# Kernel optimization log

Hardware: AMD Instinct MI355X
Metric: run time of the kernel (lower is better)

## Reference

```python
import jax, jax.numpy as jnp
import numpy as np

LN_EPS = 1e-5


def setup_inputs() -> dict:
    key = jax.random.key(0)
    ks = jax.random.split(key, 10)
    N, E, D, H = 32000, 512000, 256, 128
    atom_features = jax.random.normal(ks[0], (N, D), dtype=jnp.float32)
    edge_features = jax.random.normal(ks[1], (E, H), dtype=jnp.float32)
    edge_index = jax.random.randint(ks[2], (2, E), 0, N, dtype=jnp.int64)
    s = lambda fan_in: 1.0 / np.sqrt(fan_in)
    W_lin = jax.random.normal(ks[3], (D, H), dtype=jnp.float32) * s(D)
    W1 = jax.random.normal(ks[4], (3 * H, H), dtype=jnp.float32) * s(3 * H)
    b1 = jnp.zeros((H,), jnp.float32)
    W2 = jax.random.normal(ks[5], (H, H), dtype=jnp.float32) * s(H)
    b2 = jnp.zeros((H,), jnp.float32)
    W3 = jax.random.normal(ks[6], (H, H), dtype=jnp.float32) * s(H)
    b3 = jnp.zeros((H,), jnp.float32)
    gamma = jnp.ones((H,), jnp.float32)
    beta = jnp.zeros((H,), jnp.float32)
    return dict(atom_features=atom_features, edge_features=edge_features,
                edge_index=edge_index, W_lin=W_lin, W1=W1, b1=b1, W2=W2,
                b2=b2, W3=W3, b3=b3, gamma=gamma, beta=beta)


def _layernorm(x, gamma, beta):
    mu = jnp.mean(x, axis=-1, keepdims=True)
    var = jnp.mean((x - mu) ** 2, axis=-1, keepdims=True)
    return (x - mu) * jax.lax.rsqrt(var + LN_EPS) * gamma + beta


def reference(atom_features, edge_features, edge_index, W_lin, W1, b1, W2, b2, W3, b3, gamma, beta):
    # o3.Linear on scalar irreps -> plain bias-free linear: [N, D] @ [D, H]
    atom_scalars = atom_features @ W_lin  # [N, H]
    edge_dst, edge_src = edge_index[0], edge_index[1]
    # gather + concat: [E, 3H]
    edge_in = jnp.concatenate(
        [atom_scalars[edge_dst], atom_scalars[edge_src], edge_features], axis=-1)
    h = jax.nn.relu(edge_in @ W1 + b1)
    h = jax.nn.relu(h @ W2 + b2)
    h = h @ W3 + b3  # [E, H]
    return _layernorm(edge_features + h, gamma, beta)
```

## Files before the change

kernel.cpp:

```cpp
#include <hip/hip_runtime.h>

typedef __attribute__((ext_vector_type(8))) short bf16x8;
typedef __attribute__((ext_vector_type(16))) float f32x16;

#define LN_EPS 1e-5f

__device__ __forceinline__ unsigned short f2bf(float f) {
    unsigned u = __float_as_uint(f);
    unsigned r = (u + 0x7FFFu + ((u >> 16) & 1u)) >> 16;
    return (unsigned short)r;
}

__global__ void prep_weights(const float* __restrict__ W_lin,
                             const float* __restrict__ W1,
                             const float* __restrict__ W2,
                             const float* __restrict__ W3,
                             unsigned short* __restrict__ wt_lin,
                             unsigned short* __restrict__ wt5) {
    int i = blockIdx.x * blockDim.x + threadIdx.x;
    if (i < 128 * 256) {
        int n = i >> 8, k = i & 255;
        wt_lin[n * 256 + k] = f2bf(W_lin[k * 128 + n]);
    } else if (i < 128 * 256 + 5 * 128 * 128) {
        int j = i - 128 * 256;
        int m = j >> 14, r = j & 16383;
        int n = r >> 7, k = r & 127;
        float v;
        if (m < 3)       v = W1[(m * 128 + k) * 128 + n];
        else if (m == 3) v = W2[k * 128 + n];
        else             v = W3[k * 128 + n];
        int kk = k ^ ((n & 7) << 3);
        wt5[m * 16384 + n * 128 + kk] = f2bf(v);
    }
}

__global__ void atoms_gemm(const float* __restrict__ af,
                           const unsigned short* __restrict__ wt_lin,
                           unsigned short* __restrict__ atoms_bf,
                           int Natoms) {
    const int wv = threadIdx.x >> 6, lane = threadIdx.x & 63;
    const int l31 = lane & 31, g8 = (lane >> 5) * 8, g4 = (lane >> 5) * 4;
    const int R = blockIdx.x * 128 + wv * 32;

    f32x16 acc[4];
#pragma unroll
    for (int f = 0; f < 4; ++f)
#pragma unroll
        for (int e = 0; e < 16; ++e) acc[f][e] = 0.0f;

    int arow = R + l31;
    if (arow >= Natoms) arow = Natoms - 1;
    const float* ap = af + (size_t)arow * 256;

#pragma unroll
    for (int ks = 0; ks < 16; ++ks) {
        const int k0 = ks * 16 + g8;
        float4 x0 = *(const float4*)(ap + k0);
        float4 x1 = *(const float4*)(ap + k0 + 4);
        bf16x8 a;
        a[0] = (short)f2bf(x0.x); a[1] = (short)f2bf(x0.y);
        a[2] = (short)f2bf(x0.z); a[3] = (short)f2bf(x0.w);
        a[4] = (short)f2bf(x1.x); a[5] = (short)f2bf(x1.y);
        a[6] = (short)f2bf(x1.z); a[7] = (short)f2bf(x1.w);
#pragma unroll
        for (int f = 0; f < 4; ++f) {
            bf16x8 b = *(const bf16x8*)(wt_lin + (32 * f + l31) * 256 + k0);
            acc[f] = __builtin_amdgcn_mfma_f32_32x32x16_bf16(a, b, acc[f], 0, 0, 0);
        }
    }

#pragma unroll
    for (int f = 0; f < 4; ++f) {
        const int col = 32 * f + l31;
#pragma unroll
        for (int r = 0; r < 16; ++r) {
            int row = R + (r & 3) + 8 * (r >> 2) + g4;
            if (row < Natoms) atoms_bf[(size_t)row * 128 + col] = f2bf(acc[f][r]);
        }
    }
}

__device__ __forceinline__ void zero4(f32x16* a) {
#pragma unroll
    for (int f = 0; f < 4; ++f)
#pragma unroll
        for (int e = 0; e < 16; ++e) a[f][e] = 0.0f;
}

__device__ __forceinline__ void chunk_globalA(const unsigned short* __restrict__ arow,
                                              const unsigned short* __restrict__ W,
                                              int l31, int g8, int sw, f32x16* acc) {
#pragma unroll
    for (int ks = 0; ks < 8; ++ks) {
        bf16x8 a = *(const bf16x8*)(arow + ks * 16 + g8);
#pragma unroll
        for (int f = 0; f < 4; ++f) {
            bf16x8 b = *(const bf16x8*)(W + (32 * f + l31) * 128 + ((ks * 16 + g8) ^ sw));
            acc[f] = __builtin_amdgcn_mfma_f32_32x32x16_bf16(a, b, acc[f], 0, 0, 0);
        }
    }
}

__device__ __forceinline__ void chunk_ldsA(const unsigned short* __restrict__ actw,
                                           const unsigned short* __restrict__ W,
                                           int l31, int g8, int sw, f32x16* acc) {
#pragma unroll
    for (int ks = 0; ks < 8; ++ks) {
        bf16x8 a = *(const bf16x8*)(actw + l31 * 128 + ((ks * 16 + g8) ^ sw));
#pragma unroll
        for (int f = 0; f < 4; ++f) {
            bf16x8 b = *(const bf16x8*)(W + (32 * f + l31) * 128 + ((ks * 16 + g8) ^ sw));
            acc[f] = __builtin_amdgcn_mfma_f32_32x32x16_bf16(a, b, acc[f], 0, 0, 0);
        }
    }
}

__global__ __launch_bounds__(512, 2) void edge_mlp(
    const float* __restrict__ ef, const int* __restrict__ eidx,
    const unsigned short* __restrict__ atoms_bf,
    const unsigned short* __restrict__ wt5,
    const float* __restrict__ b1, const float* __restrict__ b2,
    const float* __restrict__ b3, const float* __restrict__ gamma_,
    const float* __restrict__ beta_, float* __restrict__ out, int E) {
    __shared__ unsigned short Wbuf[2][16384];
    __shared__ unsigned short act[8][4096];

    const int tid = threadIdx.x;
    const int wv = tid >> 6, lane = tid & 63;
    const int l31 = lane & 31, g = lane >> 5, g8 = g * 8, g4 = g * 4;
    const int sw = (l31 & 7) << 3;
    const int R = blockIdx.x * 256 + wv * 32;

    auto stage = [&](int buf, int mat) {
        const char* s = (const char*)(wt5 + mat * 16384);
        char* d = (char*)(&Wbuf[buf][0]);
        const int o = tid * 16;
#pragma unroll
        for (int i = 0; i < 4; ++i)
            __builtin_amdgcn_global_load_lds(
                (const __attribute__((address_space(1))) unsigned int*)(s + o + i * 8192),
                (__attribute__((address_space(3))) unsigned int*)(d + o + i * 8192),
                16, 0, 0);
    };

    int e_l = R + l31;
    if (e_l >= E) e_l = E - 1;
    const int dstI = eidx[e_l];
    const int srcI = eidx[E + e_l];

    float b1c[4], b2c[4], b3c[4], gc[4], bc[4];
#pragma unroll
    for (int f = 0; f < 4; ++f) {
        const int c = 32 * f + l31;
        b1c[f] = b1[c]; b2c[f] = b2[c]; b3c[f] = b3[c];
        gc[f] = gamma_[c]; bc[f] = beta_[c];
    }

    unsigned short* actw = &act[wv][0];
    f32x16 acc[4];

    stage(0, 0);
    __syncthreads();

    zero4(acc);
    stage(1, 1);
    chunk_globalA(atoms_bf + (size_t)dstI * 128, &Wbuf[0][0], l31, g8, sw, acc);
    __syncthreads();

    stage(0, 2);
    chunk_globalA(atoms_bf + (size_t)srcI * 128, &Wbuf[1][0], l31, g8, sw, acc);
    __syncthreads();

    stage(1, 3);
    {
        const float* erow = ef + (size_t)e_l * 128;
        const unsigned short* W = &Wbuf[0][0];
#pragma unroll
        for (int ks = 0; ks < 8; ++ks) {
            const int k0 = ks * 16 + g8;
            float4 x0 = *(const float4*)(erow + k0);
            float4 x1 = *(const float4*)(erow + k0 + 4);
            bf16x8 a;
            a[0] = (short)f2bf(x0.x); a[1] = (short)f2bf(x0.y);
            a[2] = (short)f2bf(x0.z); a[3] = (short)f2bf(x0.w);
            a[4] = (short)f2bf(x1.x); a[5] = (short)f2bf(x1.y);
            a[6] = (short)f2bf(x1.z); a[7] = (short)f2bf(x1.w);
#pragma unroll
            for (int f = 0; f < 4; ++f) {
                bf16x8 b = *(const bf16x8*)(W + (32 * f + l31) * 128 + (k0 ^ sw));
                acc[f] = __builtin_amdgcn_mfma_f32_32x32x16_bf16(a, b, acc[f], 0, 0, 0);
            }
        }
    }
#pragma unroll
    for (int f = 0; f < 4; ++f) {
        const int col = 32 * f + l31;
#pragma unroll
        for (int r = 0; r < 16; ++r) {
            const int row = (r & 3) + 8 * (r >> 2) + g4;
            float v = fmaxf(acc[f][r] + b1c[f], 0.0f);
            actw[row * 128 + (col ^ ((row & 7) << 3))] = f2bf(v);
        }
    }
    __syncthreads();

    stage(0, 4);
    zero4(acc);
    chunk_ldsA(actw, &Wbuf[1][0], l31, g8, sw, acc);
#pragma unroll
    for (int f = 0; f < 4; ++f) {
        const int col = 32 * f + l31;
#pragma unroll
        for (int r = 0; r < 16; ++r) {
            const int row = (r & 3) + 8 * (r >> 2) + g4;
            float v = fmaxf(acc[f][r] + b2c[f], 0.0f);
            actw[row * 128 + (col ^ ((row & 7) << 3))] = f2bf(v);
        }
    }
    __syncthreads();

    zero4(acc);
    chunk_ldsA(actw, &Wbuf[0][0], l31, g8, sw, acc);

    float s_[16], q_[16];
#pragma unroll
    for (int r = 0; r < 16; ++r) { s_[r] = 0.0f; q_[r] = 0.0f; }
#pragma unroll
    for (int f = 0; f < 4; ++f) {
#pragma unroll
        for (int r = 0; r < 16; ++r) {
            int row = R + (r & 3) + 8 * (r >> 2) + g4;
            if (row >= E) row = E - 1;
            float v = acc[f][r] + b3c[f] + ef[(size_t)row * 128 + 32 * f + l31];
            acc[f][r] = v;
            s_[r] += v;
            q_[r] += v * v;
        }
    }
#pragma unroll
    for (int m = 1; m <= 16; m <<= 1) {
#pragma unroll
        for (int r = 0; r < 16; ++r) {
            s_[r] += __shfl_xor(s_[r], m, 64);
            q_[r] += __shfl_xor(q_[r], m, 64);
        }
    }
#pragma unroll
    for (int r = 0; r < 16; ++r) {
        const float mu = s_[r] * (1.0f / 128.0f);
        const float var = q_[r] * (1.0f / 128.0f) - mu * mu;
        const float rs = rsqrtf(var + LN_EPS);
        const int row = R + (r & 3) + 8 * (r >> 2) + g4;
        if (row < E) {
#pragma unroll
            for (int f = 0; f < 4; ++f)
                out[(size_t)row * 128 + 32 * f + l31] =
                    (acc[f][r] - mu) * rs * gc[f] + bc[f];
        }
    }
}

extern "C" void kernel_launch(void* const* d_in, const int* in_sizes, int n_in,
                              void* d_out, int out_size, void* d_ws, size_t ws_size,
                              hipStream_t stream) {
    const float* atom_features = (const float*)d_in[0];
    const float* edge_features = (const float*)d_in[1];
    const int* edge_index = (const int*)d_in[2];
    const float* W_lin = (const float*)d_in[3];
    const float* W1 = (const float*)d_in[4];
    const float* b1 = (const float*)d_in[5];
    const float* W2 = (const float*)d_in[6];
    const float* b2 = (const float*)d_in[7];
    const float* W3 = (const float*)d_in[8];
    const float* b3 = (const float*)d_in[9];
    const float* gamma_ = (const float*)d_in[10];
    const float* beta_ = (const float*)d_in[11];
    float* out = (float*)d_out;

    const int Natoms = in_sizes[0] / 256;
    const int E = in_sizes[1] / 128;

    unsigned short* atoms_bf = (unsigned short*)d_ws;
    unsigned short* wt_lin = atoms_bf + (size_t)Natoms * 128;
    unsigned short* wt5 = wt_lin + 128 * 256;

    const int prep_items = 128 * 256 + 5 * 128 * 128;
    prep_weights<<<(prep_items + 255) / 256, 256, 0, stream>>>(W_lin, W1, W2, W3,
                                                               wt_lin, wt5);
    atoms_gemm<<<(Natoms + 127) / 128, 256, 0, stream>>>(atom_features, wt_lin,
                                                         atoms_bf, Natoms);
    edge_mlp<<<(E + 255) / 256, 512, 0, stream>>>(edge_features, edge_index,
                                                  atoms_bf, wt5, b1, b2, b3,
                                                  gamma_, beta_, out, E);
}
```

Before: 267.5 us.

## Transpose edge MLP so activations stay in registers, weights read from pre-tiled global image

The edge MLP now computes the transposed product, with weights as the A operand and edge rows as B. Each lane's accumulator then holds a full edge row, so inter-layer activations are rebuilt in registers using packed bf16 conversion and permlane32 swaps instead of going through LDS, and the LayerNorm reduction needs a single cross-half shuffle. Weights are pre-arranged into a fragment-ordered image and read directly from global/L2 rather than staged into LDS with barriers. Blocks shrink to 256 threads with three blocks per CU, and output stores become vectorized float4. The risks are higher register pressure and repeated global weight reads per wave.

```diff
diff --git a/kernel.cpp b/kernel.cpp
--- a/kernel.cpp
+++ b/kernel.cpp
@@ -2,6 +2,8 @@
 
 typedef __attribute__((ext_vector_type(8))) short bf16x8;
 typedef __attribute__((ext_vector_type(16))) float f32x16;
+typedef __attribute__((ext_vector_type(4))) float f32x4;
+typedef __attribute__((ext_vector_type(4))) unsigned u32x4;
 
 #define LN_EPS 1e-5f
 
@@ -9,6 +11,16 @@
     unsigned u = __float_as_uint(f);
     unsigned r = (u + 0x7FFFu + ((u >> 16) & 1u)) >> 16;
     return (unsigned short)r;
+}
+
+__device__ __forceinline__ unsigned cvt_pk_bf16(float lo, float hi) {
+    unsigned r;
+    asm("v_cvt_pk_bf16_f32 %0, %1, %2" : "=v"(r) : "v"(lo), "v"(hi));
+    return r;
+}
+
+__device__ __forceinline__ void permswap(unsigned& a, unsigned& b) {
+    asm("v_permlane32_swap_b32 %0, %1" : "+v"(a), "+v"(b));
 }
 
 __global__ void prep_weights(const float* __restrict__ W_lin,
@@ -16,21 +28,22 @@
                              const float* __restrict__ W2,
                              const float* __restrict__ W3,
                              unsigned short* __restrict__ wt_lin,
-                             unsigned short* __restrict__ wt5) {
+                             unsigned short* __restrict__ wimg) {
     int i = blockIdx.x * blockDim.x + threadIdx.x;
     if (i < 128 * 256) {
         int n = i >> 8, k = i & 255;
         wt_lin[n * 256 + k] = f2bf(W_lin[k * 128 + n]);
-    } else if (i < 128 * 256 + 5 * 128 * 128) {
+    } else if (i < 128 * 256 + 5 * 16384) {
         int j = i - 128 * 256;
-        int m = j >> 14, r = j & 16383;
-        int n = r >> 7, k = r & 127;
+        int mat = j >> 14, r = j & 16383;
+        int jj = r & 7, l = (r >> 3) & 63, ks = (r >> 9) & 7, f = r >> 12;
+        int n = 32 * f + (l & 31);
+        int k = 16 * ks + 8 * (l >> 5) + jj;
         float v;
-        if (m < 3)       v = W1[(m * 128 + k) * 128 + n];
-        else if (m == 3) v = W2[k * 128 + n];
-        else             v = W3[k * 128 + n];
-        int kk = k ^ ((n & 7) << 3);
-        wt5[m * 16384 + n * 128 + kk] = f2bf(v);
+        if (mat < 3)       v = W1[(mat * 128 + k) * 128 + n];
+        else if (mat == 3) v = W2[k * 128 + n];
+        else               v = W3[k * 128 + n];
+        wimg[j + mat * 0 + (j - r) * 0 + (mat * 16384 + r) - j] = f2bf(v);
     }
 }
 
@@ -80,183 +93,155 @@
     }
 }
 
-__device__ __forceinline__ void zero4(f32x16* a) {
-#pragma unroll
-    for (int f = 0; f < 4; ++f)
-#pragma unroll
-        for (int e = 0; e < 16; ++e) a[f][e] = 0.0f;
-}
-
-__device__ __forceinline__ void chunk_globalA(const unsigned short* __restrict__ arow,
-                                              const unsigned short* __restrict__ W,
-                                              int l31, int g8, int sw, f32x16* acc) {
-#pragma unroll
-    for (int ks = 0; ks < 8; ++ks) {
-        bf16x8 a = *(const bf16x8*)(arow + ks * 16 + g8);
-#pragma unroll
-        for (int f = 0; f < 4; ++f) {
-            bf16x8 b = *(const bf16x8*)(W + (32 * f + l31) * 128 + ((ks * 16 + g8) ^ sw));
-            acc[f] = __builtin_amdgcn_mfma_f32_32x32x16_bf16(a, b, acc[f], 0, 0, 0);
-        }
-    }
-}
-
-__device__ __forceinline__ void chunk_ldsA(const unsigned short* __restrict__ actw,
-                                           const unsigned short* __restrict__ W,
-                                           int l31, int g8, int sw, f32x16* acc) {
-#pragma unroll
-    for (int ks = 0; ks < 8; ++ks) {
-        bf16x8 a = *(const bf16x8*)(actw + l31 * 128 + ((ks * 16 + g8) ^ sw));
-#pragma unroll
-        for (int f = 0; f < 4; ++f) {
-            bf16x8 b = *(const bf16x8*)(W + (32 * f + l31) * 128 + ((ks * 16 + g8) ^ sw));
-            acc[f] = __builtin_amdgcn_mfma_f32_32x32x16_bf16(a, b, acc[f], 0, 0, 0);
-        }
-    }
-}
-
-__global__ __launch_bounds__(512, 2) void edge_mlp(
+__global__ __launch_bounds__(256, 3) void edge_fused(
     const float* __restrict__ ef, const int* __restrict__ eidx,
     const unsigned short* __restrict__ atoms_bf,
-    const unsigned short* __restrict__ wt5,
+    const unsigned short* __restrict__ wimg,
     const float* __restrict__ b1, const float* __restrict__ b2,
     const float* __restrict__ b3, const float* __restrict__ gamma_,
     const float* __restrict__ beta_, float* __restrict__ out, int E) {
-    __shared__ unsigned short Wbuf[2][16384];
-    __shared__ unsigned short act[8][4096];
-
-    const int tid = threadIdx.x;
-    const int wv = tid >> 6, lane = tid & 63;
-    const int l31 = lane & 31, g = lane >> 5, g8 = g * 8, g4 = g * 4;
-    const int sw = (l31 & 7) << 3;
-    const int R = blockIdx.x * 256 + wv * 32;
-
-    auto stage = [&](int buf, int mat) {
-        const char* s = (const char*)(wt5 + mat * 16384);
-        char* d = (char*)(&Wbuf[buf][0]);
-        const int o = tid * 16;
-#pragma unroll
-        for (int i = 0; i < 4; ++i)
-            __builtin_amdgcn_global_load_lds(
-                (const __attribute__((address_space(1))) unsigned int*)(s + o + i * 8192),
-                (__attribute__((address_space(3))) unsigned int*)(d + o + i * 8192),
-                16, 0, 0);
+    const int lane = threadIdx.x & 63;
+    const int wv = threadIdx.x >> 6;
+    const int l31 = lane & 31;
+    const int hi = lane >> 5;
+    const int h8 = hi * 8;
+
+    const int e0 = blockIdx.x * 128 + wv * 32 + l31;
+    const int e = e0 < E ? e0 : E - 1;
+    const int dstI = eidx[e];
+    const int srcI = eidx[E + e];
+    const unsigned short* dstRow = atoms_bf + (size_t)dstI * 128;
+    const unsigned short* srcRow = atoms_bf + (size_t)srcI * 128;
+    const float* efRow = ef + (size_t)e * 128;
+
+    const unsigned short* wbase = wimg + lane * 8;
+
+    f32x16 acc[4];
+
+    auto initb = [&](const float* __restrict__ bb) {
+#pragma unroll
+        for (int f = 0; f < 4; ++f)
+#pragma unroll
+            for (int m = 0; m < 4; ++m) {
+                f32x4 b4 = *(const f32x4*)(bb + 32 * f + 8 * m + 4 * hi);
+#pragma unroll
+                for (int i = 0; i < 4; ++i) acc[f][4 * m + i] = b4[i];
+            }
     };
 
-    int e_l = R + l31;
-    if (e_l >= E) e_l = E - 1;
-    const int dstI = eidx[e_l];
-    const int srcI = eidx[E + e_l];
-
-    float b1c[4], b2c[4], b3c[4], gc[4], bc[4];
-#pragma unroll
-    for (int f = 0; f < 4; ++f) {
-        const int c = 32 * f + l31;
-        b1c[f] = b1[c]; b2c[f] = b2[c]; b3c[f] = b3[c];
-        gc[f] = gamma_[c]; bc[f] = beta_[c];
-    }
-
-    unsigned short* actw = &act[wv][0];
-    f32x16 acc[4];
-
-    stage(0, 0);
-    __syncthreads();
-
-    zero4(acc);
-    stage(1, 1);
-    chunk_globalA(atoms_bf + (size_t)dstI * 128, &Wbuf[0][0], l31, g8, sw, acc);
-    __syncthreads();
-
-    stage(0, 2);
-    chunk_globalA(atoms_bf + (size_t)srcI * 128, &Wbuf[1][0], l31, g8, sw, acc);
-    __syncthreads();
-
-    stage(1, 3);
-    {
-        const float* erow = ef + (size_t)e_l * 128;
-        const unsigned short* W = &Wbuf[0][0];
-#pragma unroll
-        for (int ks = 0; ks < 8; ++ks) {
-            const int k0 = ks * 16 + g8;
-            float4 x0 = *(const float4*)(erow + k0);
-            float4 x1 = *(const float4*)(erow + k0 + 4);
-            bf16x8 a;
-            a[0] = (short)f2bf(x0.x); a[1] = (short)f2bf(x0.y);
-            a[2] = (short)f2bf(x0.z); a[3] = (short)f2bf(x0.w);
-            a[4] = (short)f2bf(x1.x); a[5] = (short)f2bf(x1.y);
-            a[6] = (short)f2bf(x1.z); a[7] = (short)f2bf(x1.w);
-#pragma unroll
-            for (int f = 0; f < 4; ++f) {
-                bf16x8 b = *(const bf16x8*)(W + (32 * f + l31) * 128 + (k0 ^ sw));
-                acc[f] = __builtin_amdgcn_mfma_f32_32x32x16_bf16(a, b, acc[f], 0, 0, 0);
-            }
-        }
-    }
-#pragma unroll
-    for (int f = 0; f < 4; ++f) {
-        const int col = 32 * f + l31;
-#pragma unroll
-        for (int r = 0; r < 16; ++r) {
-            const int row = (r & 3) + 8 * (r >> 2) + g4;
-            float v = fmaxf(acc[f][r] + b1c[f], 0.0f);
-            actw[row * 128 + (col ^ ((row & 7) << 3))] = f2bf(v);
-        }
-    }
-    __syncthreads();
-
-    stage(0, 4);
-    zero4(acc);
-    chunk_ldsA(actw, &Wbuf[1][0], l31, g8, sw, acc);
-#pragma unroll
-    for (int f = 0; f < 4; ++f) {
-        const int col = 32 * f + l31;
-#pragma unroll
-        for (int r = 0; r < 16; ++r) {
-            const int row = (r & 3) + 8 * (r >> 2) + g4;
-            float v = fmaxf(acc[f][r] + b2c[f], 0.0f);
-            actw[row * 128 + (col ^ ((row & 7) << 3))] = f2bf(v);
-        }
-    }
-    __syncthreads();
-
-    zero4(acc);
-    chunk_ldsA(actw, &Wbuf[0][0], l31, g8, sw, acc);
-
-    float s_[16], q_[16];
-#pragma unroll
-    for (int r = 0; r < 16; ++r) { s_[r] = 0.0f; q_[r] = 0.0f; }
-#pragma unroll
-    for (int f = 0; f < 4; ++f) {
-#pragma unroll
-        for (int r = 0; r < 16; ++r) {
-            int row = R + (r & 3) + 8 * (r >> 2) + g4;
-            if (row >= E) row = E - 1;
-            float v = acc[f][r] + b3c[f] + ef[(size_t)row * 128 + 32 * f + l31];
-            acc[f][r] = v;
-            s_[r] += v;
-            q_[r] += v * v;
-        }
-    }
-#pragma unroll
-    for (int m = 1; m <= 16; m <<= 1) {
-#pragma unroll
-        for (int r = 0; r < 16; ++r) {
-            s_[r] += __shfl_xor(s_[r], m, 64);
-            q_[r] += __shfl_xor(q_[r], m, 64);
-        }
-    }
-#pragma unroll
-    for (int r = 0; r < 16; ++r) {
-        const float mu = s_[r] * (1.0f / 128.0f);
-        const float var = q_[r] * (1.0f / 128.0f) - mu * mu;
-        const float rs = rsqrtf(var + LN_EPS);
-        const int row = R + (r & 3) + 8 * (r >> 2) + g4;
-        if (row < E) {
-#pragma unroll
-            for (int f = 0; f < 4; ++f)
-                out[(size_t)row * 128 + 32 * f + l31] =
-                    (acc[f][r] - mu) * rs * gc[f] + bc[f];
-        }
+    bf16x8 frag[8];
+    auto build_frags = [&]() {
+#pragma unroll
+        for (int f = 0; f < 4; ++f) {
+            unsigned pk0[4], pk1[4];
+#pragma unroll
+            for (int m = 0; m < 4; ++m) {
+                float a0 = fmaxf(acc[f][4 * m + 0], 0.0f);
+                float a1 = fmaxf(acc[f][4 * m + 1], 0.0f);
+                float a2 = fmaxf(acc[f][4 * m + 2], 0.0f);
+                float a3 = fmaxf(acc[f][4 * m + 3], 0.0f);
+                pk0[m] = cvt_pk_bf16(a0, a1);
+                pk1[m] = cvt_pk_bf16(a2, a3);
+            }
+#pragma unroll
+            for (int k1 = 0; k1 < 2; ++k1) {
+                unsigned x0 = pk0[2 * k1], y0 = pk0[2 * k1 + 1];
+                unsigned x1 = pk1[2 * k1], y1 = pk1[2 * k1 + 1];
+                permswap(x0, y0);
+                permswap(x1, y1);
+                union { u32x4 u; bf16x8 b; } cv;
+                cv.u = (u32x4){x0, x1, y0, y1};
+                frag[2 * f + k1] = cv.b;
+            }
+        }
+    };
+
+    initb(b1);
+#pragma unroll
+    for (int ks = 0; ks < 8; ++ks) {
+        bf16x8 bx = *(const bf16x8*)(dstRow + ks * 16 + h8);
+#pragma unroll
+        for (int f = 0; f < 4; ++f) {
+            bf16x8 a = *(const bf16x8*)(wbase + ((0 * 4 + f) * 8 + ks) * 512);
+            acc[f] = __builtin_amdgcn_mfma_f32_32x32x16_bf16(a, bx, acc[f], 0, 0, 0);
+        }
+    }
+#pragma unroll
+    for (int ks = 0; ks < 8; ++ks) {
+        bf16x8 bx = *(const bf16x8*)(srcRow + ks * 16 + h8);
+#pragma unroll
+        for (int f = 0; f < 4; ++f) {
+            bf16x8 a = *(const bf16x8*)(wbase + ((1 * 4 + f) * 8 + ks) * 512);
+            acc[f] = __builtin_amdgcn_mfma_f32_32x32x16_bf16(a, bx, acc[f], 0, 0, 0);
+        }
+    }
+#pragma unroll
+    for (int ks = 0; ks < 8; ++ks) {
+        f32x4 x0 = *(const f32x4*)(efRow + ks * 16 + h8);
+        f32x4 x1 = *(const f32x4*)(efRow + ks * 16 + h8 + 4);
+        union { u32x4 u; bf16x8 b; } cv;
+        cv.u = (u32x4){cvt_pk_bf16(x0[0], x0[1]), cvt_pk_bf16(x0[2], x0[3]),
+                       cvt_pk_bf16(x1[0], x1[1]), cvt_pk_bf16(x1[2], x1[3])};
+#pragma unroll
+        for (int f = 0; f < 4; ++f) {
+            bf16x8 a = *(const bf16x8*)(wbase + ((2 * 4 + f) * 8 + ks) * 512);
+            acc[f] = __builtin_amdgcn_mfma_f32_32x32x16_bf16(a, cv.b, acc[f], 0, 0, 0);
+        }
+    }
+
+    build_frags();
+    initb(b2);
+#pragma unroll
+    for (int ks = 0; ks < 8; ++ks)
+#pragma unroll
+        for (int f = 0; f < 4; ++f) {
+            bf16x8 a = *(const bf16x8*)(wbase + ((3 * 4 + f) * 8 + ks) * 512);
+            acc[f] = __builtin_amdgcn_mfma_f32_32x32x16_bf16(a, frag[ks], acc[f], 0, 0, 0);
+        }
+
+    build_frags();
+    initb(b3);
+#pragma unroll
+    for (int ks = 0; ks < 8; ++ks)
+#pragma unroll
+        for (int f = 0; f < 4; ++f) {
+            bf16x8 a = *(const bf16x8*)(wbase + ((4 * 4 + f) * 8 + ks) * 512);
+            acc[f] = __builtin_amdgcn_mfma_f32_32x32x16_bf16(a, frag[ks], acc[f], 0, 0, 0);
+        }
+
+    float s = 0.0f, q = 0.0f;
+#pragma unroll
+    for (int f = 0; f < 4; ++f)
+#pragma unroll
+        for (int m = 0; m < 4; ++m) {
+            f32x4 r4 = *(const f32x4*)(efRow + 32 * f + 8 * m + 4 * hi);
+#pragma unroll
+            for (int i = 0; i < 4; ++i) {
+                float v = acc[f][4 * m + i] + r4[i];
+                acc[f][4 * m + i] = v;
+                s += v;
+                q += v * v;
+            }
+        }
+    s += __shfl_xor(s, 32, 64);
+    q += __shfl_xor(q, 32, 64);
+    const float mu = s * (1.0f / 128.0f);
+    const float var = q * (1.0f / 128.0f) - mu * mu;
+    const float rs = rsqrtf(var + LN_EPS);
+
+    if (e0 < E) {
+#pragma unroll
+        for (int f = 0; f < 4; ++f)
+#pragma unroll
+            for (int m = 0; m < 4; ++m) {
+                f32x4 g4 = *(const f32x4*)(gamma_ + 32 * f + 8 * m + 4 * hi);
+                f32x4 be4 = *(const f32x4*)(beta_ + 32 * f + 8 * m + 4 * hi);
+                f32x4 o;
+#pragma unroll
+                for (int i = 0; i < 4; ++i)
+                    o[i] = (acc[f][4 * m + i] - mu) * rs * g4[i] + be4[i];
+                *(f32x4*)(out + (size_t)e * 128 + 32 * f + 8 * m + 4 * hi) = o;
+            }
     }
 }
 
@@ -282,14 +267,14 @@
 
     unsigned short* atoms_bf = (unsigned short*)d_ws;
     unsigned short* wt_lin = atoms_bf + (size_t)Natoms * 128;
-    unsigned short* wt5 = wt_lin + 128 * 256;
-
-    const int prep_items = 128 * 256 + 5 * 128 * 128;
+    unsigned short* wimg = wt_lin + 128 * 256;
+
+    const int prep_items = 128 * 256 + 5 * 16384;
     prep_weights<<<(prep_items + 255) / 256, 256, 0, stream>>>(W_lin, W1, W2, W3,
-                                                               wt_lin, wt5);
+                                                               wt_lin, wimg);
     atoms_gemm<<<(Natoms + 127) / 128, 256, 0, stream>>>(atom_features, wt_lin,
                                                          atoms_bf, Natoms);
-    edge_mlp<<<(E + 255) / 256, 512, 0, stream>>>(edge_features, edge_index,
-                                                  atoms_bf, wt5, b1, b2, b3,
-                                                  gamma_, beta_, out, E);
-}
+    edge_fused<<<(E + 127) / 128, 256, 0, stream>>>(edge_features, edge_index,
+                                                    atoms_bf, wimg, b1, b2, b3,
+                                                    gamma_, beta_, out, E);
+}
```

Result: slower. 390.8 us (+46.1%).
